# Kernel tuning notes

Hardware: AMD Instinct MI355X
Metric: run time of the kernel (lower is better)

The kernel has to match this reference:

```python
import jax, jax.numpy as jnp
import numpy as np

N = 200000        # total nodes
NPL = 12500       # nodes per topological level
NLVL = 16         # number of topological levels (N = NPL*NLVL)
DEG = 8           # avg in-degree for nodes in levels >= 1
IN_DIM = 128
H = 128           # per-direction hidden (unidirectional -> hidden_dim)
LAYERS = 2


def setup_inputs() -> dict:
    rng = np.random.default_rng(0)
    feats = jnp.asarray(rng.standard_normal((N, IN_DIM)).astype(np.float32))
    stdv = 1.0 / np.sqrt(H)
    wx = jnp.asarray(rng.uniform(-stdv, stdv, (IN_DIM + (LAYERS - 1) * H, 1, 3 * H)).astype(np.float32))
    wh = jnp.asarray(rng.uniform(-stdv, stdv, (LAYERS, H, 1, 3 * H)).astype(np.float32))
    b = jnp.asarray(rng.uniform(-stdv, stdv, (LAYERS, 1, 3 * H)).astype(np.float32))
    # DAG edges grouped by destination level; src is any node in an earlier level
    srcs, dsts = [], []
    for lvl in range(1, NLVL):
        dst = np.repeat(np.arange(lvl * NPL, (lvl + 1) * NPL, dtype=np.int32), DEG)
        src = rng.integers(0, lvl * NPL, size=NPL * DEG).astype(np.int32)
        srcs.append(src)
        dsts.append(dst)
    edge_src = jnp.asarray(np.concatenate(srcs))
    edge_dst = jnp.asarray(np.concatenate(dsts))
    index_map = jnp.arange(N, dtype=jnp.int32)
    return dict(features=feats, weights_x=wx, weights_h=wh, biases=b,
                edge_src=edge_src, edge_dst=edge_dst, index_map=index_map,
                num_levels=NLVL, nodes_per_level=NPL)


def _daggru(features, weights_x, weights_h, biases, edge_src, edge_dst,
            index_map, num_levels, nodes_per_level):
    n_nodes, in_dim = features.shape
    layers, hd = weights_h.shape[0], weights_h.shape[1]
    npl = nodes_per_level
    epl = edge_src.shape[0] // (num_levels - 1)  # edges per level block
    # h = zeros.index_add_(0, index_map, features)
    x = jnp.zeros_like(features).at[index_map].add(features)
    row = 0
    h = None
    for layer in range(layers):
        rows = in_dim if layer == 0 else hd
        Wx = weights_x[row:row + rows, 0]          # [rows, 3H]
        row += rows
        Wh = weights_h[layer, :, 0]                # [H, 3H]
        b = biases[layer, 0]                       # [3H]
        gx = x @ Wx + b                            # [N, 3H] precomputed input gates
        h = jnp.zeros((n_nodes, hd), dtype=features.dtype)
        for lvl in range(num_levels):
            s = lvl * npl
            if lvl == 0:
                m = jnp.zeros((npl, hd), dtype=features.dtype)
            else:
                es = edge_src[(lvl - 1) * epl: lvl * epl]
                ed = edge_dst[(lvl - 1) * epl: lvl * epl] - s
                m = jax.ops.segment_sum(h[es], ed, num_segments=npl)
                deg = jax.ops.segment_sum(jnp.ones((epl,), features.dtype), ed, num_segments=npl)
                m = m / jnp.maximum(deg, 1.0)[:, None]   # in-degree normalization
            g = gx[s:s + npl]
            gh = m @ Wh
            r = jax.nn.sigmoid(g[:, :hd] + gh[:, :hd])
            z = jax.nn.sigmoid(g[:, hd:2 * hd] + gh[:, hd:2 * hd])
            n = jnp.tanh(g[:, 2 * hd:] + r * gh[:, 2 * hd:])
            h = h.at[s:s + npl].set((1.0 - z) * n + z * m)
        x = h
    return h[index_map]


def reference(features, weights_x, weights_h, biases, edge_src, edge_dst,
              index_map, num_levels, nodes_per_level):
    return _daggru(features, weights_x, weights_h, biases, edge_src, edge_dst,
                   index_map, num_levels, nodes_per_level)
```

## Files before the change

### kernel.cpp

```cpp
#include <hip/hip_runtime.h>
#include <stdint.h>

#define N_NODES 200000
#define NPL     12500
#define NLVL    16
#define DEG     8
#define EPL     (NPL*DEG)
#define HD      128
#define KTOT    256
#define MT      32
#define NBLK    391
#define ASTR    264
#define WTL     98304

typedef unsigned short u16;
typedef unsigned int   u32;

typedef __attribute__((ext_vector_type(8)))  short  short8;
typedef __attribute__((ext_vector_type(16))) float  f32x16;

__device__ __forceinline__ float bf2f(u32 u) { return __uint_as_float(u << 16); }
__device__ __forceinline__ float bflo(u32 u) { return __uint_as_float(u << 16); }
__device__ __forceinline__ float bfhi(u32 u) { return __uint_as_float(u & 0xFFFF0000u); }
__device__ __forceinline__ u16 f2bf(float f) {
  u32 u = __float_as_uint(f);
  return (u16)((u + 0x7FFFu + ((u >> 16) & 1u)) >> 16);
}
__device__ __forceinline__ u32 pack2(float a, float b) {
  u32 ua = __float_as_uint(a), ub = __float_as_uint(b);
  ua = (ua + 0x7FFFu + ((ua >> 16) & 1u)) >> 16;
  ub = ((ub + 0x7FFFu + ((ub >> 16) & 1u)) >> 16) << 16;
  return ua | ub;
}
__device__ __forceinline__ float fsig(float x) {
  return __builtin_amdgcn_rcpf(1.f + __builtin_amdgcn_exp2f(-1.4426950408889634f * x));
}
__device__ __forceinline__ float ftanh(float x) {
  float t = __builtin_amdgcn_exp2f(2.8853900817779268f * x);
  return 1.f - 2.f * __builtin_amdgcn_rcpf(t + 1.f);
}

__global__ __launch_bounds__(256) void scatter_x(const float* __restrict__ f,
    const int* __restrict__ idx, u16* __restrict__ xb)
{
  const int t = blockIdx.x * 256 + threadIdx.x;
  const int i = t >> 4, sg = (t & 15) * 8;
  const int d = idx[i];
  const float4 a = *(const float4*)(f + (size_t)i * HD + sg);
  const float4 b = *(const float4*)(f + (size_t)i * HD + sg + 4);
  uint4 o;
  o.x = pack2(a.x, a.y); o.y = pack2(a.z, a.w);
  o.z = pack2(b.x, b.y); o.w = pack2(b.z, b.w);
  *(uint4*)(xb + (size_t)d * HD + sg) = o;
}

__global__ __launch_bounds__(256) void gather_out(const u16* __restrict__ hb,
    const int* __restrict__ idx, float* __restrict__ o)
{
  const int t = blockIdx.x * 256 + threadIdx.x;
  const int i = t >> 4, sg = (t & 15) * 8;
  const int s = idx[i];
  const uint4 v = *(const uint4*)(hb + (size_t)s * HD + sg);
  float4 lo, hi;
  lo.x = bflo(v.x); lo.y = bfhi(v.x); lo.z = bflo(v.y); lo.w = bfhi(v.y);
  hi.x = bflo(v.z); hi.y = bfhi(v.z); hi.z = bflo(v.w); hi.w = bfhi(v.w);
  *(float4*)(o + (size_t)i * HD + sg)     = lo;
  *(float4*)(o + (size_t)i * HD + sg + 4) = hi;
}

__global__ __launch_bounds__(256) void build_wt(const float* __restrict__ wx,
    const float* __restrict__ wh, u16* __restrict__ wt)
{
  const int t = blockIdx.x * 256 + threadIdx.x;
  const int l = t / WTL;
  const int r = t - l * WTL;
  const int e = r & 7;
  const int chunk = r >> 3;
  const int lane = chunk & 63;
  const int tile = chunk >> 6;
  const int l31 = lane & 31, lq = lane >> 5;
  int col, k;
  if (tile < 128)      { col =       (tile >> 4) * 32 + l31; k =       (tile & 15) * 16 + lq * 8 + e; }
  else if (tile < 160) { col = 256 + ((tile - 128) >> 3) * 32 + l31; k = ((tile - 128) & 7) * 16 + lq * 8 + e; }
  else                 { col = 384 + ((tile - 160) >> 3) * 32 + l31; k = 128 + ((tile - 160) & 7) * 16 + lq * 8 + e; }
  float v;
  if (col < 384) {
    v = (k < 128) ? wx[(size_t)(l * 128 + k) * 384 + col]
                  : wh[(size_t)l * 49152 + (size_t)(k - 128) * 384 + col];
  } else {
    v = wh[(size_t)l * 49152 + (size_t)(k - 128) * 384 + (col - 128)];
  }
  wt[(size_t)l * WTL + r] = f2bf(v);
}

__global__ __launch_bounds__(256, 4) void level_step(
    u16* __restrict__ bufA, u16* __restrict__ bufB,
    const u16* __restrict__ wt, const float* __restrict__ bias,
    const int* __restrict__ esrc, int stage)
{
  __shared__ __align__(16) u16 sA[MT * ASTR];

  int blk = blockIdx.x, layer, lvl;
  if (blk < NBLK) { layer = 0; lvl = stage; }
  else            { layer = 1; lvl = stage - 1; blk -= NBLK; }
  if (lvl < 0 || lvl >= NLVL) return;

  const u16*   x  = layer ? bufB : bufA;
  u16*         h  = layer ? bufA : bufB;
  const u16*   Wt = wt  + (size_t)layer * WTL;
  const float* bs = bias + (size_t)layer * 384;

  const int tid = threadIdx.x;

  {
    const int sub = tid >> 4;
    const int c8  = (tid & 15) * 8;
    uint4 z4; z4.x = z4.y = z4.z = z4.w = 0u;
    #pragma unroll
    for (int it = 0; it < 2; ++it) {
      const int row  = it * 16 + sub;
      const int lrow = blk * MT + row;
      const bool valid = (lrow < NPL);
      uint4* dx = (uint4*)(sA + row * ASTR + c8);
      *dx = valid ? *(const uint4*)(x + (size_t)(lvl * NPL + lrow) * HD + c8) : z4;
      uint4* dm = (uint4*)(sA + row * ASTR + HD + c8);
      if (lvl > 0 && valid) {
        const int eb = (lvl - 1) * EPL + lrow * DEG;
        const int4 e0 = *(const int4*)(esrc + eb);
        const int4 e1 = *(const int4*)(esrc + eb + 4);
        const int srcs[8] = { e0.x, e0.y, e0.z, e0.w, e1.x, e1.y, e1.z, e1.w };
        float acc[8];
        #pragma unroll
        for (int i = 0; i < 8; ++i) acc[i] = 0.f;
        #pragma unroll
        for (int e = 0; e < 8; ++e) {
          const uint4 v = *(const uint4*)(h + (size_t)srcs[e] * HD + c8);
          acc[0] += bflo(v.x); acc[1] += bfhi(v.x);
          acc[2] += bflo(v.y); acc[3] += bfhi(v.y);
          acc[4] += bflo(v.z); acc[5] += bfhi(v.z);
          acc[6] += bflo(v.w); acc[7] += bfhi(v.w);
        }
        uint4 o;
        o.x = pack2(acc[0] * 0.125f, acc[1] * 0.125f);
        o.y = pack2(acc[2] * 0.125f, acc[3] * 0.125f);
        o.z = pack2(acc[4] * 0.125f, acc[5] * 0.125f);
        o.w = pack2(acc[6] * 0.125f, acc[7] * 0.125f);
        *dm = o;
      } else {
        *dm = z4;
      }
    }
  }
  __syncthreads();

  const int wv = tid >> 6, lane = tid & 63;
  const int l31 = lane & 31, lq = lane >> 5;

  f32x16 acc[4];
  {
    const float b0 = bs[      32 * wv + l31];
    const float b1 = bs[128 + 32 * wv + l31];
    const float b2 = bs[256 + 32 * wv + l31];
    #pragma unroll
    for (int r = 0; r < 16; ++r) {
      acc[0][r] = b0; acc[1][r] = b1; acc[2][r] = b2; acc[3][r] = 0.f;
    }
  }

  const u16* wlane = Wt + (size_t)lane * 8;
  #pragma unroll
  for (int t = 0; t < 16; ++t) {
    const short8 a0  = *(const short8*)(sA + l31 * ASTR + t * 16 + lq * 8);
    const short8 bb0 = *(const short8*)(wlane + (size_t)((wv    ) * 16 + t) * 512);
    const short8 bb1 = *(const short8*)(wlane + (size_t)((wv + 4) * 16 + t) * 512);
    acc[0] = __builtin_amdgcn_mfma_f32_32x32x16_bf16(a0, bb0, acc[0], 0, 0, 0);
    acc[1] = __builtin_amdgcn_mfma_f32_32x32x16_bf16(a0, bb1, acc[1], 0, 0, 0);
    if (t < 8) {
      const short8 bb2 = *(const short8*)(wlane + (size_t)(128 + wv * 8 + t) * 512);
      acc[2] = __builtin_amdgcn_mfma_f32_32x32x16_bf16(a0, bb2, acc[2], 0, 0, 0);
    } else {
      const short8 bb3 = *(const short8*)(wlane + (size_t)(160 + wv * 8 + (t - 8)) * 512);
      acc[3] = __builtin_amdgcn_mfma_f32_32x32x16_bf16(a0, bb3, acc[3], 0, 0, 0);
    }
  }

  const int jcol = 32 * wv + l31;
  #pragma unroll
  for (int r = 0; r < 16; ++r) {
    const int rowe = (r & 3) + 8 * (r >> 2) + 4 * lq;
    const int lrow = blk * MT + rowe;
    if (lrow < NPL) {
      const float gr  = acc[0][r];
      const float gz  = acc[1][r];
      const float gxn = acc[2][r];
      const float ghn = acc[3][r];
      const float mv  = bf2f(sA[rowe * ASTR + HD + jcol]);
      const float rg  = fsig(gr);
      const float zg  = fsig(gz);
      const float ng  = ftanh(gxn + rg * ghn);
      const float hv  = (1.f - zg) * ng + zg * mv;
      h[(size_t)(lvl * NPL + lrow) * HD + jcol] = f2bf(hv);
    }
  }
}

extern "C" void kernel_launch(void* const* d_in, const int* in_sizes, int n_in,
                              void* d_out, int out_size, void* d_ws, size_t ws_size,
                              hipStream_t stream)
{
  (void)in_sizes; (void)n_in; (void)out_size; (void)ws_size;
  const float* feats = (const float*)d_in[0];
  const float* wx    = (const float*)d_in[1];
  const float* wh    = (const float*)d_in[2];
  const float* bias  = (const float*)d_in[3];
  const int*   esrc  = (const int*)d_in[4];
  const int*   imap  = (const int*)d_in[6];
  float* out = (float*)d_out;

  char* ws = (char*)d_ws;
  u16* bufA = (u16*)ws;
  u16* bufB = (u16*)(ws + 51200000);
  u16* wt   = (u16*)(ws + 102400000);

  scatter_x<<<12500, 256, 0, stream>>>(feats, imap, bufA);
  build_wt<<<768, 256, 0, stream>>>(wx, wh, wt);

  for (int stage = 0; stage <= NLVL; ++stage)
    level_step<<<2 * NBLK, 256, 0, stream>>>(bufA, bufB, wt, bias, esrc, stage);

  gather_out<<<12500, 256, 0, stream>>>(bufA, imap, out);
}
```

Measured before the change: 538.6 us.

## Pre-aggregate older-level neighbor sums one stage ahead in concurrent blocks

Adds extra blocks to each stage launch that sum neighbor hidden states from levels older than the previous one into an fp32 double-buffered partial-sum workspace, for the next stage's levels. The main blocks then only gather sources from the immediately preceding level and add the stored partial. The aim is to shorten the dependent gather on the critical path by overlapping most of it with the previous stage's GEMM work. The cost is extra fp32 partial-sum traffic and more blocks per launch, and the new path depends on the workspace size being sufficient.

```diff
diff --git a/kernel.cpp b/kernel.cpp
--- a/kernel.cpp
+++ b/kernel.cpp
@@ -10,6 +10,7 @@
 #define KTOT    256
 #define MT      32
 #define NBLK    391
+#define PB      782
 #define ASTR    264
 #define WTL     98304
 
@@ -93,6 +94,160 @@
   wt[(size_t)l * WTL + r] = f2bf(v);
 }
 
+__global__ __launch_bounds__(256, 4) void level_step_pg(
+    u16* __restrict__ bufA, u16* __restrict__ bufB,
+    const u16* __restrict__ wt, const float* __restrict__ bias,
+    const int* __restrict__ esrc, float* __restrict__ mAcc, int stage)
+{
+  __shared__ __align__(16) u16 sA[MT * ASTR];
+  const int tid = threadIdx.x;
+  const int blk0 = blockIdx.x;
+
+  if (blk0 >= 2 * NBLK) {
+    const int pb   = blk0 - 2 * NBLK;
+    const int L    = (pb < PB) ? 0 : 1;
+    const int pblk = L ? (pb - PB) : pb;
+    const int tlvl = L ? stage : stage + 1;
+    if (tlvl < 1 || tlvl >= NLVL) return;
+    const int row = pblk * 16 + (tid >> 4);
+    if (row >= NPL) return;
+    const int c8 = (tid & 15) * 8;
+    const int cutoff = (tlvl - 1) * NPL;
+    const u16* hs = L ? bufA : bufB;
+    const int eb = (tlvl - 1) * EPL + row * DEG;
+    const int4 e0 = *(const int4*)(esrc + eb);
+    const int4 e1 = *(const int4*)(esrc + eb + 4);
+    const int srcs[8] = { e0.x, e0.y, e0.z, e0.w, e1.x, e1.y, e1.z, e1.w };
+    float acc[8];
+    #pragma unroll
+    for (int i = 0; i < 8; ++i) acc[i] = 0.f;
+    #pragma unroll
+    for (int e = 0; e < 8; ++e) {
+      if (srcs[e] < cutoff) {
+        const uint4 v = *(const uint4*)(hs + (size_t)srcs[e] * HD + c8);
+        acc[0] += bflo(v.x); acc[1] += bfhi(v.x);
+        acc[2] += bflo(v.y); acc[3] += bfhi(v.y);
+        acc[4] += bflo(v.z); acc[5] += bfhi(v.z);
+        acc[6] += bflo(v.w); acc[7] += bfhi(v.w);
+      }
+    }
+    float* mp = mAcc + ((size_t)((((stage + 1) & 1) * 2) + L) * NPL + row) * HD + c8;
+    float4 o0, o1;
+    o0.x = acc[0]; o0.y = acc[1]; o0.z = acc[2]; o0.w = acc[3];
+    o1.x = acc[4]; o1.y = acc[5]; o1.z = acc[6]; o1.w = acc[7];
+    *(float4*)(mp)     = o0;
+    *(float4*)(mp + 4) = o1;
+    return;
+  }
+
+  int blk = blk0, layer, lvl;
+  if (blk < NBLK) { layer = 0; lvl = stage; }
+  else            { layer = 1; lvl = stage - 1; blk -= NBLK; }
+  if (lvl < 0 || lvl >= NLVL) return;
+
+  const u16*   x  = layer ? bufB : bufA;
+  u16*         h  = layer ? bufA : bufB;
+  const u16*   Wt = wt  + (size_t)layer * WTL;
+  const float* bs = bias + (size_t)layer * 384;
+
+  {
+    const int sub = tid >> 4;
+    const int c8  = (tid & 15) * 8;
+    uint4 z4; z4.x = z4.y = z4.z = z4.w = 0u;
+    #pragma unroll
+    for (int it = 0; it < 2; ++it) {
+      const int row  = it * 16 + sub;
+      const int lrow = blk * MT + row;
+      const bool valid = (lrow < NPL);
+      uint4* dx = (uint4*)(sA + row * ASTR + c8);
+      *dx = valid ? *(const uint4*)(x + (size_t)(lvl * NPL + lrow) * HD + c8) : z4;
+      uint4* dm = (uint4*)(sA + row * ASTR + HD + c8);
+      if (lvl > 0 && valid) {
+        const int cutoff = (lvl - 1) * NPL;
+        const float* mp = mAcc + ((size_t)(((stage & 1) * 2) + layer) * NPL + lrow) * HD + c8;
+        const float4 p0 = *(const float4*)(mp);
+        const float4 p1 = *(const float4*)(mp + 4);
+        float acc[8];
+        acc[0] = p0.x; acc[1] = p0.y; acc[2] = p0.z; acc[3] = p0.w;
+        acc[4] = p1.x; acc[5] = p1.y; acc[6] = p1.z; acc[7] = p1.w;
+        const int eb = (lvl - 1) * EPL + lrow * DEG;
+        const int4 e0 = *(const int4*)(esrc + eb);
+        const int4 e1 = *(const int4*)(esrc + eb + 4);
+        const int srcs[8] = { e0.x, e0.y, e0.z, e0.w, e1.x, e1.y, e1.z, e1.w };
+        #pragma unroll
+        for (int e = 0; e < 8; ++e) {
+          if (srcs[e] >= cutoff) {
+            const uint4 v = *(const uint4*)(h + (size_t)srcs[e] * HD + c8);
+            acc[0] += bflo(v.x); acc[1] += bfhi(v.x);
+            acc[2] += bflo(v.y); acc[3] += bfhi(v.y);
+            acc[4] += bflo(v.z); acc[5] += bfhi(v.z);
+            acc[6] += bflo(v.w); acc[7] += bfhi(v.w);
+          }
+        }
+        uint4 o;
+        o.x = pack2(acc[0] * 0.125f, acc[1] * 0.125f);
+        o.y = pack2(acc[2] * 0.125f, acc[3] * 0.125f);
+        o.z = pack2(acc[4] * 0.125f, acc[5] * 0.125f);
+        o.w = pack2(acc[6] * 0.125f, acc[7] * 0.125f);
+        *dm = o;
+      } else {
+        *dm = z4;
+      }
+    }
+  }
+  __syncthreads();
+
+  const int wv = tid >> 6, lane = tid & 63;
+  const int l31 = lane & 31, lq = lane >> 5;
+
+  f32x16 acc[4];
+  {
+    const float b0 = bs[      32 * wv + l31];
+    const float b1 = bs[128 + 32 * wv + l31];
+    const float b2 = bs[256 + 32 * wv + l31];
+    #pragma unroll
+    for (int r = 0; r < 16; ++r) {
+      acc[0][r] = b0; acc[1][r] = b1; acc[2][r] = b2; acc[3][r] = 0.f;
+    }
+  }
+
+  const u16* wlane = Wt + (size_t)lane * 8;
+  #pragma unroll
+  for (int t = 0; t < 16; ++t) {
+    const short8 a0  = *(const short8*)(sA + l31 * ASTR + t * 16 + lq * 8);
+    const short8 bb0 = *(const short8*)(wlane + (size_t)((wv    ) * 16 + t) * 512);
+    const short8 bb1 = *(const short8*)(wlane + (size_t)((wv + 4) * 16 + t) * 512);
+    acc[0] = __builtin_amdgcn_mfma_f32_32x32x16_bf16(a0, bb0, acc[0], 0, 0, 0);
+    acc[1] = __builtin_amdgcn_mfma_f32_32x32x16_bf16(a0, bb1, acc[1], 0, 0, 0);
+    if (t < 8) {
+      const short8 bb2 = *(const short8*)(wlane + (size_t)(128 + wv * 8 + t) * 512);
+      acc[2] = __builtin_amdgcn_mfma_f32_32x32x16_bf16(a0, bb2, acc[2], 0, 0, 0);
+    } else {
+      const short8 bb3 = *(const short8*)(wlane + (size_t)(160 + wv * 8 + (t - 8)) * 512);
+      acc[3] = __builtin_amdgcn_mfma_f32_32x32x16_bf16(a0, bb3, acc[3], 0, 0, 0);
+    }
+  }
+
+  const int jcol = 32 * wv + l31;
+  #pragma unroll
+  for (int r = 0; r < 16; ++r) {
+    const int rowe = (r & 3) + 8 * (r >> 2) + 4 * lq;
+    const int lrow = blk * MT + rowe;
+    if (lrow < NPL) {
+      const float gr  = acc[0][r];
+      const float gz  = acc[1][r];
+      const float gxn = acc[2][r];
+      const float ghn = acc[3][r];
+      const float mv  = bf2f(sA[rowe * ASTR + HD + jcol]);
+      const float rg  = fsig(gr);
+      const float zg  = fsig(gz);
+      const float ng  = ftanh(gxn + rg * ghn);
+      const float hv  = (1.f - zg) * ng + zg * mv;
+      h[(size_t)(lvl * NPL + lrow) * HD + jcol] = f2bf(hv);
+    }
+  }
+}
+
 __global__ __launch_bounds__(256, 4) void level_step(
     u16* __restrict__ bufA, u16* __restrict__ bufB,
     const u16* __restrict__ wt, const float* __restrict__ bias,
@@ -111,7 +266,6 @@
   const float* bs = bias + (size_t)layer * 384;
 
   const int tid = threadIdx.x;
-
   {
     const int sub = tid >> 4;
     const int c8  = (tid & 15) * 8;
@@ -208,7 +362,7 @@
                               void* d_out, int out_size, void* d_ws, size_t ws_size,
                               hipStream_t stream)
 {
-  (void)in_sizes; (void)n_in; (void)out_size; (void)ws_size;
+  (void)in_sizes; (void)n_in; (void)out_size;
   const float* feats = (const float*)d_in[0];
   const float* wx    = (const float*)d_in[1];
   const float* wh    = (const float*)d_in[2];
@@ -221,12 +375,21 @@
   u16* bufA = (u16*)ws;
   u16* bufB = (u16*)(ws + 51200000);
   u16* wt   = (u16*)(ws + 102400000);
+  const size_t MACC_OFF = 102793216;
+  const size_t WS_NEED  = MACC_OFF + 2ull * 2ull * NPL * HD * 4ull;
 
   scatter_x<<<12500, 256, 0, stream>>>(feats, imap, bufA);
   build_wt<<<768, 256, 0, stream>>>(wx, wh, wt);
 
-  for (int stage = 0; stage <= NLVL; ++stage)
-    level_step<<<2 * NBLK, 256, 0, stream>>>(bufA, bufB, wt, bias, esrc, stage);
+  if (ws_size >= WS_NEED) {
+    float* mAcc = (float*)(ws + MACC_OFF);
+    for (int stage = 0; stage <= NLVL; ++stage)
+      level_step_pg<<<2 * NBLK + 2 * PB, 256, 0, stream>>>(
+          bufA, bufB, wt, bias, esrc, mAcc, stage);
+  } else {
+    for (int stage = 0; stage <= NLVL; ++stage)
+      level_step<<<2 * NBLK, 256, 0, stream>>>(bufA, bufB, wt, bias, esrc, stage);
+  }
 
   gather_out<<<12500, 256, 0, stream>>>(bufA, imap, out);
 }
```

Measured after the change: 584.2 us. 8.5% more time.
